# Kernel tuning notes

Hardware: AMD Instinct MI355X
Metric: run time of the kernel (lower is better)

Reference implementation:

```python
import jax, jax.numpy as jnp
import numpy as np

N_NODES = 20000
N_EDGES = 100000
WALK_LEN = 4
FEAT_DIM = 256
HID = 64
NUM_HEAD = 8
H_RNN = NUM_HEAD * HID  # 512
OUT_DIM = 16


def setup_inputs() -> dict:
    key = jax.random.key(0)
    ks = jax.random.split(key, 12)
    s = 0.05  # small init scale for numerical stability
    return {
        "x": jax.random.normal(ks[0], (N_NODES, FEAT_DIM), jnp.float32),
        "W_mlp": jax.random.normal(ks[1], (HID, FEAT_DIM), jnp.float32) * s,
        "b_mlp": jnp.zeros((HID,), jnp.float32),
        "W_ih": jax.random.normal(ks[2], (3 * H_RNN, HID), jnp.float32) * s,
        "W_hh": jax.random.normal(ks[3], (3 * H_RNN, H_RNN), jnp.float32) * s,
        "b_ih": jnp.zeros((3 * H_RNN,), jnp.float32),
        "b_hh": jnp.zeros((3 * H_RNN,), jnp.float32),
        "attn": jax.random.normal(ks[4], (1, NUM_HEAD, HID), jnp.float32) * s,
        "W_emb": jax.random.normal(ks[5], (HID, H_RNN), jnp.float32) * s,
        "b_emb": jnp.zeros((HID,), jnp.float32),
        "W_last": jax.random.normal(ks[6], (OUT_DIM, HID), jnp.float32) * s,
        "b_last": jnp.zeros((OUT_DIM,), jnp.float32),
        "edge_metapath_indices": jax.random.randint(ks[7], (N_EDGES, WALK_LEN), 0, N_NODES),
        "num_nodes": N_NODES,
    }


def reference(x, W_mlp, b_mlp, W_ih, W_hh, b_ih, b_hh, attn, W_emb, b_emb,
              W_last, b_last, edge_metapath_indices, num_nodes):
    # self channel: embedding = mlp(data.x)
    emb = x @ W_mlp.T + b_mlp                       # [N, hid]

    # rnn channel: gather per-metapath node embeddings
    edata = emb[edge_metapath_indices]              # [E, L, hid]
    E = edata.shape[0]
    h_rnn = W_hh.shape[1]

    # torch nn.GRU cell (gate order r, z, n), scan over path length
    def gru_step(h, x_t):
        xg = x_t @ W_ih.T + b_ih                    # [E, 3H]
        hg = h @ W_hh.T + b_hh                      # [E, 3H]
        xr, xz, xn = jnp.split(xg, 3, axis=-1)
        hr, hz, hn = jnp.split(hg, 3, axis=-1)
        r = jax.nn.sigmoid(xr + hr)
        z = jax.nn.sigmoid(xz + hz)
        n = jnp.tanh(xn + r * hn)
        return (1.0 - z) * n + z * h, None

    h0 = jnp.zeros((E, h_rnn), edata.dtype)
    hT, _ = jax.lax.scan(gru_step, h0, jnp.swapaxes(edata, 0, 1))  # [E, 8*hid]

    num_head, hid = attn.shape[1], attn.shape[2]
    eft = hT.reshape(E, num_head, hid)              # per-edge features

    # attention logits + leaky_relu(0.01)
    a = jnp.sum(eft * attn, axis=-1)                # [E, num_head]
    a = jnp.where(a > 0, a, 0.01 * a)

    # edge softmax grouped by destination node (indices[:, -1])
    dst = edge_metapath_indices[:, -1]
    m = jax.ops.segment_max(a, dst, num_segments=num_nodes)        # [N, H]
    ea = jnp.exp(a - m[dst])
    ssum = jax.ops.segment_sum(ea, dst, num_segments=num_nodes)    # [N, H]
    alpha = ea / ssum[dst]                          # [E, H]

    # message passing: scatter-sum of attention-weighted edge features
    ft = jax.ops.segment_sum(eft * alpha[:, :, None], dst,
                             num_segments=num_nodes)               # [N, H, hid]
    ret = ft.reshape(num_nodes, num_head * hid)
    rnn_emb = ret @ W_emb.T + b_emb                 # [N, hid]

    out = rnn_emb @ W_last.T + b_last               # [N, out_dim]
    return out
```

## Files before the change

### kernel.cpp

```cpp
#include <hip/hip_runtime.h>
#include <hip/hip_bf16.h>
#include <cstdint>

#define N_NODES 20000
#define N_EDGES 100000
#define WALK 4
#define FDIM 256
#define HID 64
#define NHEAD 8
#define HR 512
#define OUTD 16

typedef __attribute__((ext_vector_type(8))) short bf16x8;
typedef __attribute__((ext_vector_type(8))) unsigned short u16x8;
typedef __attribute__((ext_vector_type(4))) float f32x4;

__device__ __forceinline__ float b2f(unsigned short u){
  union{float f; unsigned u;} x; x.u = ((unsigned)u)<<16; return x.f;
}
__device__ __forceinline__ unsigned short f2b(float f){
  union{float f; unsigned u;} x; x.f = f;
  unsigned r = x.u + 0x7FFFu + ((x.u>>16)&1u);
  return (unsigned short)(r>>16);
}
__device__ __forceinline__ float sigmoidf_(float v){ return 1.0f/(1.0f+__expf(-v)); }
__device__ __forceinline__ float tanh_c(float v){
  v = fminf(fmaxf(v, -15.f), 15.f);
  const float t2 = __expf(2.0f*v);
  return (t2 - 1.0f) / (t2 + 1.0f);
}

__device__ __forceinline__ void gload16(const void* g, void* l){
  __builtin_amdgcn_global_load_lds(
      (const __attribute__((address_space(1))) void*)(g),
      (__attribute__((address_space(3))) void*)(l),
      16, 0, 0);
}

__device__ __forceinline__ f32x4 mfma16(bf16x8 a, bf16x8 b, f32x4 c){
  return __builtin_amdgcn_mfma_f32_16x16x32_bf16(a, b, c, 0, 0, 0);
}

__launch_bounds__(256)
__global__ void emb_kernel(const float* __restrict__ x,
                           const float* __restrict__ Wm,
                           const float* __restrict__ bm,
                           unsigned short* __restrict__ emb_bf)
{
  __shared__ float xs[4][FDIM];
  const int tid = threadIdx.x;
  const int node0 = blockIdx.x * 4;
  {
    const int row = tid >> 6;
    const int k4  = (tid & 63) * 4;
    *reinterpret_cast<float4*>(&xs[row][k4]) =
      *reinterpret_cast<const float4*>(&x[(size_t)(node0+row)*FDIM + k4]);
  }
  __syncthreads();
  const int nn = tid >> 6, c = tid & 63;
  float acc = bm[c];
  const float* wr = &Wm[c*FDIM];
  #pragma unroll 8
  for (int k=0;k<FDIM;k+=4){
    const float4 w = *reinterpret_cast<const float4*>(&wr[k]);
    acc += xs[nn][k]*w.x + xs[nn][k+1]*w.y + xs[nn][k+2]*w.z + xs[nn][k+3]*w.w;
  }
  emb_bf[(size_t)(node0+nn)*HID + c] = f2b(acc);
}

__launch_bounds__(256)
__global__ void prep_kernel(const float* __restrict__ Whh,
                            const float* __restrict__ Wih,
                            const float* __restrict__ Wemb,
                            unsigned short* __restrict__ WhhP,
                            unsigned short* __restrict__ WihP,
                            unsigned short* __restrict__ WembP)
{
  const int t = blockIdx.x*256 + threadIdx.x;
  if (t < 8*192*512){
    const int k = t & 511;
    const int r = (t >> 9) % 192;
    const int db = t / 98304;
    const int G = (r>>6)*HR + db*64 + (r&63);
    const int kg = k >> 6, kw = k & 63;
    const int c = kw >> 3, o = kw & 7;
    const int ksrc = (kg<<6) + (((c ^ (r&7)) << 3) | o);
    WhhP[t] = f2b(Whh[(size_t)G*HR + ksrc]);
  }
  if (t < 8*192*64){
    const int k = t & 63;
    const int r = (t >> 6) % 192;
    const int db = t / 12288;
    const int G = (r>>6)*HR + db*64 + (r&63);
    const int c = k >> 3, o = k & 7;
    const int ksrc = (((c ^ (r&7)) << 3) | o);
    WihP[t] = f2b(Wih[(size_t)G*HID + ksrc]);
  }
  if (t < 64*512){
    const int k = t & 511;
    const int o = t >> 9;
    const int kg = k >> 6, kw = k & 63;
    const int c = kw >> 3, off = kw & 7;
    const int ksrc = (kg<<6) + (((c ^ (o&7)) << 3) | off);
    WembP[t] = f2b(Wemb[(size_t)o*HR + ksrc]);
  }
}

__launch_bounds__(256)
__global__ void xg_kernel(const unsigned short* __restrict__ emb_bf,
                          const unsigned short* __restrict__ WihP,
                          const float* __restrict__ b_ih,
                          const float* __restrict__ b_hh,
                          unsigned short* __restrict__ xnP,
                          unsigned short* __restrict__ h1n)
{
  __shared__ __align__(16) unsigned short As[128*64];
  __shared__ __align__(16) unsigned short Bs[192*64];
  const int tid = threadIdx.x, lane = tid & 63, w = tid >> 6;
  const int tx = lane & 15, ty = lane >> 4;
  const int n0 = blockIdx.x * 128;
  const int db = blockIdx.y;

  #pragma unroll
  for (int j=0;j<4;++j){
    const int flat = j*256 + tid;
    const int row = flat >> 3, c = flat & 7;
    int n = n0 + row; if (n > N_NODES-1) n = N_NODES-1;
    gload16(emb_bf + ((size_t)n*HID + ((c ^ (row&7))<<3)), (char*)As + flat*16);
  }
  #pragma unroll
  for (int j=0;j<6;++j){
    const int flat = j*256 + tid;
    const int row = flat >> 3, c = flat & 7;
    gload16(WihP + ((size_t)(db*192 + row)*HID + c*8), (char*)Bs + flat*16);
  }
  __syncthreads();

  f32x4 acc[2][12];
  #pragma unroll
  for (int m=0;m<2;++m)
    #pragma unroll
    for (int f=0;f<12;++f) acc[m][f] = (f32x4)(0.f);

  auto readFrag = [&](const unsigned short* base, int row, int kk)->bf16x8{
    const int chunk = (kk<<2) + ty;
    return *reinterpret_cast<const bf16x8*>(
        reinterpret_cast<const char*>(base) + (row<<7) + ((chunk ^ (row&7))<<4));
  };
  #pragma unroll
  for (int kk=0; kk<2; ++kk){
    const bf16x8 a0 = readFrag(As, w*32 + tx, kk);
    const bf16x8 a1 = readFrag(As, w*32 + 16 + tx, kk);
    #pragma unroll
    for (int nf=0; nf<12; ++nf){
      const bf16x8 b = readFrag(Bs, nf*16 + tx, kk);
      acc[0][nf] = mfma16(a0, b, acc[0][nf]);
      acc[1][nf] = mfma16(a1, b, acc[1][nf]);
    }
  }

  #pragma unroll
  for (int m=0;m<2;++m){
    #pragma unroll
    for (int reg=0; reg<4; ++reg){
      const int row = w*32 + m*16 + ty*4 + reg;
      const int n = n0 + row;
      if (n < N_NODES){
        #pragma unroll
        for (int fr=0; fr<4; ++fr){
          const int d6 = fr*16 + tx;
          const int dG = db*64 + d6;
          const float xr = acc[m][fr][reg]   + b_ih[dG];
          const float xz = acc[m][4+fr][reg] + b_ih[HR+dG];
          const float xn = acc[m][8+fr][reg] + b_ih[2*HR+dG];
          xnP[((size_t)db*N_NODES + n)*64 + d6] = f2b(xn);
          const float r = sigmoidf_(xr + b_hh[dG]);
          const float z = sigmoidf_(xz + b_hh[HR+dG]);
          const float nn = tanh_c(xn + r*b_hh[2*HR+dG]);
          h1n[(size_t)n*HR + dG] = f2b((1.0f - z)*nn);
        }
      }
    }
  }
}

template<int STEP, bool SCORE>
__launch_bounds__(256)
__global__ void gru_mfma(const unsigned short* __restrict__ emb_bf,
                         const int* __restrict__ idx,
                         const unsigned short* __restrict__ h_in,
                         unsigned short* __restrict__ h_out,
                         const unsigned short* __restrict__ WhhP,
                         const unsigned short* __restrict__ WihP,
                         const unsigned short* __restrict__ xnP,
                         const float* __restrict__ b_ih,
                         const float* __restrict__ b_hh,
                         const float* __restrict__ attn,
                         float* __restrict__ a_buf)
{
  constexpr bool GATHER = (STEP == 1);
  __shared__ __align__(16) unsigned short As[128*64];
  __shared__ __align__(16) unsigned short Bs[192*64];

  const int tid = threadIdx.x, lane = tid & 63, w = tid >> 6;
  const int tx = lane & 15, ty = lane >> 4;

  const int bid = blockIdx.x;
  const int sid = (bid & 7)*782 + (bid >> 3);
  const int et = sid >> 3;
  const int db = sid & 7;
  const int e0 = et * 128;

  int eS[4], nH[4], nX[4];
  #pragma unroll
  for (int j=0;j<4;++j){
    int e = e0 + ((j*256 + tid) >> 3);
    if (e > N_EDGES-1) e = N_EDGES-1;
    eS[j] = e;
    nX[j] = idx[e*WALK + STEP];
    nH[j] = GATHER ? idx[e*WALK] : 0;
  }

  f32x4 acc[2][12];
  #pragma unroll
  for (int m=0;m<2;++m)
    #pragma unroll
    for (int f=0;f<12;++f) acc[m][f] = (f32x4)(0.f);

  auto stageA = [&](int kt){
    #pragma unroll
    for (int j=0;j<4;++j){
      const int flat = j*256 + tid;
      const int row = flat >> 3, c = flat & 7;
      const unsigned short* src;
      if (kt == 8){
        src = emb_bf + ((size_t)nX[j]*HID + ((c ^ (row&7)) << 3));
      } else if (GATHER){
        src = h_in + ((size_t)nH[j]*HR + kt*64 + ((c ^ (row&7)) << 3));
      } else {
        src = h_in + ((size_t)eS[j]*HR + kt*64 + c*8);
      }
      gload16(src, (char*)As + flat*16);
    }
  };
  auto stageB = [&](int kt){
    #pragma unroll
    for (int j=0;j<6;++j){
      const int flat = j*256 + tid;
      const int row = flat >> 3, c = flat & 7;
      const unsigned short* src = (kt < 8)
        ? WhhP + ((size_t)(db*192 + row)*HR + kt*64 + c*8)
        : WihP + ((size_t)(db*192 + row)*HID + c*8);
      gload16(src, (char*)Bs + flat*16);
    }
  };
  auto readFrag = [&](const unsigned short* base, int row, int kk)->bf16x8{
    const int chunk = (kk<<2) + ty;
    return *reinterpret_cast<const bf16x8*>(
        reinterpret_cast<const char*>(base) + (row<<7) + ((chunk ^ (row&7))<<4));
  };

  stageA(0); stageB(0);

  #pragma unroll
  for (int kt=0; kt<9; ++kt){
    __syncthreads();
    #pragma unroll
    for (int kk=0; kk<2; ++kk){
      const bf16x8 a0 = readFrag(As, w*32 + tx, kk);
      const bf16x8 a1 = readFrag(As, w*32 + 16 + tx, kk);
      #pragma unroll
      for (int nf=0; nf<12; ++nf){
        if (kt == 8 && nf >= 8) continue;
        const bf16x8 b = readFrag(Bs, nf*16 + tx, kk);
        acc[0][nf] = mfma16(a0, b, acc[0][nf]);
        acc[1][nf] = mfma16(a1, b, acc[1][nf]);
      }
    }
    if (kt < 8){
      __syncthreads();
      stageA(kt+1); stageB(kt+1);
    }
  }

  float bir[4], biz[4], bhn[4], atv[4];
  #pragma unroll
  for (int fr=0; fr<4; ++fr){
    const int dG = db*64 + fr*16 + tx;
    bir[fr] = b_ih[dG]      + b_hh[dG];
    biz[fr] = b_ih[HR+dG]   + b_hh[HR+dG];
    bhn[fr] = b_hh[2*HR+dG];
    atv[fr] = SCORE ? attn[dG] : 0.f;
  }

  #pragma unroll
  for (int m=0;m<2;++m){
    #pragma unroll
    for (int reg=0; reg<4; ++reg){
      const int row = w*32 + m*16 + ty*4 + reg;
      const int e = e0 + row;
      float sp = 0.f;
      if (e < N_EDGES){
        const int nodeS = idx[e*WALK + STEP];
        const int nodeH = GATHER ? idx[e*WALK] : 0;
        #pragma unroll
        for (int fr=0; fr<4; ++fr){
          const int d6 = fr*16 + tx;
          const int dG = db*64 + d6;
          const float xn = b2f(xnP[((size_t)db*N_NODES + nodeS)*64 + d6]);
          float hold;
          if (GATHER) hold = b2f(h_in[(size_t)nodeH*HR + dG]);
          else        hold = b2f(h_in[(size_t)e*HR + db*64 + (((d6>>3) ^ (e&7))<<3) + (d6&7)]);
          const float r  = sigmoidf_(acc[m][fr][reg]   + bir[fr]);
          const float z  = sigmoidf_(acc[m][4+fr][reg] + biz[fr]);
          const float nn = tanh_c(xn + r*(acc[m][8+fr][reg] + bhn[fr]));
          const float hv = (1.0f - z)*nn + z*hold;
          h_out[(size_t)e*HR + db*64 + (((d6>>3) ^ (e&7))<<3) + (d6&7)] = f2b(hv);
          if (SCORE) sp += hv * atv[fr];
        }
      }
      if (SCORE){
        sp += __shfl_xor(sp, 1);
        sp += __shfl_xor(sp, 2);
        sp += __shfl_xor(sp, 4);
        sp += __shfl_xor(sp, 8);
        if (tx == 0 && e < N_EDGES) a_buf[e*NHEAD + db] = sp;
      }
    }
  }
}

__launch_bounds__(256)
__global__ void score2_kernel(const int* __restrict__ idx,
                              float* __restrict__ a_buf,
                              unsigned int* __restrict__ mmax)
{
  const int flat = blockIdx.x*256 + threadIdx.x;
  const int e = flat >> 3, h = flat & 7;
  const float s = a_buf[flat];
  const float a = s > 0.f ? s : 0.01f*s;
  a_buf[flat] = a;
  const int dst = idx[e*WALK + 3];
  union{float f; unsigned u;} x; x.f = a;
  const unsigned key = (x.u & 0x80000000u) ? ~x.u : (x.u | 0x80000000u);
  atomicMax(&mmax[dst*NHEAD + h], key);
}

__launch_bounds__(256)
__global__ void ea_kernel(const int* __restrict__ idx,
                          float* __restrict__ a_buf,
                          const unsigned int* __restrict__ mmax,
                          float* __restrict__ ssum)
{
  const int flat = blockIdx.x*256 + threadIdx.x;
  const int e = flat >> 3, h = flat & 7;
  const int dst = idx[e*WALK + 3];
  const unsigned key = mmax[dst*NHEAD + h];
  union{float f; unsigned u;} x;
  x.u = (key & 0x80000000u) ? (key & 0x7FFFFFFFu) : ~key;
  const float ea = __expf(a_buf[flat] - x.f);
  a_buf[flat] = ea;
  atomicAdd(&ssum[dst*NHEAD + h], ea);
}

__launch_bounds__(256)
__global__ void z_kernel(const unsigned short* __restrict__ hT,
                         const int* __restrict__ idx,
                         const float* __restrict__ ea_buf,
                         const float* __restrict__ ssum,
                         const unsigned short* __restrict__ WembP,
                         float* __restrict__ zacc)
{
  __shared__ __align__(16) char zs[40960];
  char* Az = zs;
  char* Bz = zs + 32768;
  const int tid = threadIdx.x;
  const int lane = tid & 63;
  const int w = tid >> 6;
  const int e0 = blockIdx.x * 256;

  int ej[8], dstj[8];
  #pragma unroll
  for (int j=0;j<8;++j){
    int e = e0 + ((j*256 + tid) >> 3);
    if (e > N_EDGES-1) e = N_EDGES-1;
    ej[j] = e;
    dstj[j] = idx[e*WALK + 3];
  }

  f32x4 acc[4][4];
  #pragma unroll
  for (int m=0;m<4;++m)
    #pragma unroll
    for (int f=0;f<4;++f) acc[m][f] = (f32x4)(0.f);

  auto readFrag = [&](const char* base, int row, int kk)->bf16x8{
    const int chunk = (kk<<2) + (lane>>4);
    return *reinterpret_cast<const bf16x8*>(base + (row<<7) + ((chunk ^ (row&7))<<4));
  };

  #pragma unroll 1
  for (int kt=0; kt<8; ++kt){
    __syncthreads();
    #pragma unroll
    for (int j=0;j<8;++j){
      const int flat = j*256 + tid;
      const int e = ej[j];
      const u16x8 hv = *reinterpret_cast<const u16x8*>(hT + (size_t)e*HR + kt*64 + (flat&7)*8);
      const float al = ea_buf[e*NHEAD + kt] / ssum[dstj[j]*NHEAD + kt];
      union { bf16x8 v; unsigned short s[8]; } o;
      #pragma unroll
      for (int i=0;i<8;++i) o.s[i] = f2b(b2f(hv[i]) * al);
      *reinterpret_cast<bf16x8*>(Az + flat*16) = o.v;
    }
    #pragma unroll
    for (int j=0;j<2;++j){
      const int flat = j*256 + tid;
      const int row = flat >> 3, c = flat & 7;
      gload16(WembP + ((size_t)row*HR + kt*64 + c*8), Bz + ((j*256 + w*64)<<4));
    }
    __syncthreads();
    #pragma unroll
    for (int kk=0; kk<2; ++kk){
      bf16x8 a_[4];
      #pragma unroll
      for (int mf=0; mf<4; ++mf)
        a_[mf] = readFrag(Az, w*64 + mf*16 + (lane&15), kk);
      #pragma unroll
      for (int nf=0; nf<4; ++nf){
        const bf16x8 b_ = readFrag(Bz, nf*16 + (lane&15), kk);
        #pragma unroll
        for (int mf=0; mf<4; ++mf)
          acc[mf][nf] = mfma16(a_[mf], b_, acc[mf][nf]);
      }
    }
  }

  #pragma unroll
  for (int mf=0; mf<4; ++mf){
    #pragma unroll
    for (int reg=0; reg<4; ++reg){
      const int row = w*64 + mf*16 + ((lane>>4)<<2) + reg;
      const int e = e0 + row;
      if (e < N_EDGES){
        const int dst = idx[e*WALK + 3];
        #pragma unroll
        for (int nf=0; nf<4; ++nf){
          const int o = nf*16 + (lane&15);
          atomicAdd(&zacc[(size_t)dst*64 + o], acc[mf][nf][reg]);
        }
      }
    }
  }
}

__launch_bounds__(256)
__global__ void out2_kernel(const float* __restrict__ zacc,
                            const float* __restrict__ b_emb,
                            const float* __restrict__ W_last,
                            const float* __restrict__ b_last,
                            float* __restrict__ out)
{
  const int flat = blockIdx.x*256 + threadIdx.x;
  if (flat >= N_NODES*OUTD) return;
  const int n = flat >> 4, o = flat & 15;
  float s = b_last[o];
  const float* zr = &zacc[(size_t)n*64];
  const float* wl = &W_last[o*64];
  #pragma unroll
  for (int k=0;k<64;++k) s += (zr[k] + b_emb[k]) * wl[k];
  out[(size_t)n*OUTD + o] = s;
}

extern "C" void kernel_launch(void* const* d_in, const int* in_sizes, int n_in,
                              void* d_out, int out_size, void* d_ws, size_t ws_size,
                              hipStream_t stream)
{
  (void)in_sizes; (void)n_in; (void)out_size; (void)ws_size;
  const float* x      = (const float*)d_in[0];
  const float* W_mlp  = (const float*)d_in[1];
  const float* b_mlp  = (const float*)d_in[2];
  const float* W_ih   = (const float*)d_in[3];
  const float* W_hh   = (const float*)d_in[4];
  const float* b_ih   = (const float*)d_in[5];
  const float* b_hh   = (const float*)d_in[6];
  const float* attn   = (const float*)d_in[7];
  const float* W_emb  = (const float*)d_in[8];
  const float* b_emb  = (const float*)d_in[9];
  const float* W_last = (const float*)d_in[10];
  const float* b_last = (const float*)d_in[11];
  const int*   idx    = (const int*)d_in[12];
  float* out = (float*)d_out;

  char* ws = (char*)d_ws;
  unsigned short* WhhP   = (unsigned short*)(ws + 0);
  unsigned short* WihP   = (unsigned short*)(ws + 1572864);
  unsigned short* WembP  = (unsigned short*)(ws + 1769472);
  unsigned short* emb_bf = (unsigned short*)(ws + 1835008);
  unsigned short* xnP    = (unsigned short*)(ws + 4395008);
  float*          a_buf  = (float*)(ws + 24875008);
  unsigned int*   mmax   = (unsigned int*)(ws + 28075008);
  float*          ssum   = (float*)(ws + 28715008);
  float*          zacc   = (float*)(ws + 29355008);
  unsigned short* h_a    = (unsigned short*)(ws + 34475008);
  unsigned short* h_b    = (unsigned short*)(ws + 136875008);
  unsigned short* h1n    = h_b;

  hipMemsetAsync(a_buf, 0, 9600000, stream);

  prep_kernel<<<3072, 256, 0, stream>>>(W_hh, W_ih, W_emb, WhhP, WihP, WembP);
  emb_kernel<<<N_NODES/4, 256, 0, stream>>>(x, W_mlp, b_mlp, emb_bf);

  dim3 xgrid((N_NODES + 127)/128, 8);
  xg_kernel<<<xgrid, 256, 0, stream>>>(emb_bf, WihP, b_ih, b_hh, xnP, h1n);

  const int NWG = 782*8;
  gru_mfma<1,false><<<NWG, 256, 0, stream>>>(emb_bf, idx, h1n, h_a, WhhP, WihP, xnP, b_ih, b_hh, attn, a_buf);
  gru_mfma<2,false><<<NWG, 256, 0, stream>>>(emb_bf, idx, h_a, h_b, WhhP, WihP, xnP, b_ih, b_hh, attn, a_buf);
  gru_mfma<3,true ><<<NWG, 256, 0, stream>>>(emb_bf, idx, h_b, h_a, WhhP, WihP, xnP, b_ih, b_hh, attn, a_buf);

  score2_kernel<<<N_EDGES*NHEAD/256, 256, 0, stream>>>(idx, a_buf, mmax);
  ea_kernel<<<N_EDGES*NHEAD/256, 256, 0, stream>>>(idx, a_buf, mmax, ssum);
  z_kernel<<<391, 256, 0, stream>>>(h_a, idx, a_buf, ssum, WembP, zacc);
  out2_kernel<<<(N_NODES*OUTD+255)/256, 256, 0, stream>>>(zacc, b_emb, W_last, b_last, out);
}
```

Baseline: 1.184 ms.

## Reorder gate weight rows and retile GRU MFMA to 2x2 wave grid

Permutes packed W_hh/W_ih rows so that each 16-row fragment group interleaves the r, z and n gates for the same hidden slice. The GRU step kernels then split the 128x192 tile across waves as 2x2 (64 rows by 96 columns) instead of 4x1, which cuts redundant B-fragment LDS reads per wave. The attention partial score is now accumulated with atomicAdd because two waves each contribute half of the head's dot product. xg_kernel moves to 512 threads with 256-node tiles. The cost is extra atomics and higher register pressure from the 4x6 accumulator layout.

```diff
diff --git a/kernel.cpp b/kernel.cpp
--- a/kernel.cpp
+++ b/kernel.cpp
@@ -81,7 +81,9 @@
     const int k = t & 511;
     const int r = (t >> 9) % 192;
     const int db = t / 98304;
-    const int G = (r>>6)*HR + db*64 + (r&63);
+    const int f = r >> 4, fr = r & 15;
+    const int g = f % 3, dgrp = f / 3;
+    const int G = g*HR + db*64 + dgrp*16 + fr;
     const int kg = k >> 6, kw = k & 63;
     const int c = kw >> 3, o = kw & 7;
     const int ksrc = (kg<<6) + (((c ^ (r&7)) << 3) | o);
@@ -91,7 +93,9 @@
     const int k = t & 63;
     const int r = (t >> 6) % 192;
     const int db = t / 12288;
-    const int G = (r>>6)*HR + db*64 + (r&63);
+    const int f = r >> 4, fr = r & 15;
+    const int g = f % 3, dgrp = f / 3;
+    const int G = g*HR + db*64 + dgrp*16 + fr;
     const int c = k >> 3, o = k & 7;
     const int ksrc = (((c ^ (r&7)) << 3) | o);
     WihP[t] = f2b(Wih[(size_t)G*HID + ksrc]);
@@ -106,7 +110,7 @@
   }
 }
 
-__launch_bounds__(256)
+__launch_bounds__(512)
 __global__ void xg_kernel(const unsigned short* __restrict__ emb_bf,
                           const unsigned short* __restrict__ WihP,
                           const float* __restrict__ b_ih,
@@ -114,65 +118,68 @@
                           unsigned short* __restrict__ xnP,
                           unsigned short* __restrict__ h1n)
 {
-  __shared__ __align__(16) unsigned short As[128*64];
-  __shared__ __align__(16) unsigned short Bs[192*64];
+  __shared__ __align__(16) char smem[32768 + 24576];
+  char* Ab = smem;
+  char* Bb = smem + 32768;
   const int tid = threadIdx.x, lane = tid & 63, w = tid >> 6;
-  const int tx = lane & 15, ty = lane >> 4;
-  const int n0 = blockIdx.x * 128;
+  const int wr = w >> 1, wn = w & 1;
+  const int n0 = blockIdx.x * 256;
   const int db = blockIdx.y;
 
   #pragma unroll
   for (int j=0;j<4;++j){
-    const int flat = j*256 + tid;
+    const int flat = j*512 + tid;
     const int row = flat >> 3, c = flat & 7;
     int n = n0 + row; if (n > N_NODES-1) n = N_NODES-1;
-    gload16(emb_bf + ((size_t)n*HID + ((c ^ (row&7))<<3)), (char*)As + flat*16);
-  }
-  #pragma unroll
-  for (int j=0;j<6;++j){
-    const int flat = j*256 + tid;
+    gload16(emb_bf + ((size_t)n*HID + ((c ^ (row&7))<<3)), Ab + ((j*512 + w*64)<<4));
+  }
+  #pragma unroll
+  for (int j=0;j<3;++j){
+    const int flat = j*512 + tid;
     const int row = flat >> 3, c = flat & 7;
-    gload16(WihP + ((size_t)(db*192 + row)*HID + c*8), (char*)Bs + flat*16);
-  }
-  __syncthreads();
-
-  f32x4 acc[2][12];
-  #pragma unroll
-  for (int m=0;m<2;++m)
-    #pragma unroll
-    for (int f=0;f<12;++f) acc[m][f] = (f32x4)(0.f);
-
-  auto readFrag = [&](const unsigned short* base, int row, int kk)->bf16x8{
-    const int chunk = (kk<<2) + ty;
-    return *reinterpret_cast<const bf16x8*>(
-        reinterpret_cast<const char*>(base) + (row<<7) + ((chunk ^ (row&7))<<4));
+    gload16(WihP + ((size_t)(db*192 + row)*HID + c*8), Bb + ((j*512 + w*64)<<4));
+  }
+  asm volatile("s_waitcnt vmcnt(0)" ::: "memory");
+  __builtin_amdgcn_s_barrier();
+
+  f32x4 acc[4][6];
+  #pragma unroll
+  for (int m=0;m<4;++m)
+    #pragma unroll
+    for (int f=0;f<6;++f) acc[m][f] = (f32x4)(0.f);
+
+  auto readFrag = [&](const char* base, int row, int kk)->bf16x8{
+    const int chunk = (kk<<2) + (lane>>4);
+    return *reinterpret_cast<const bf16x8*>(base + (row<<7) + ((chunk ^ (row&7))<<4));
   };
   #pragma unroll
   for (int kk=0; kk<2; ++kk){
-    const bf16x8 a0 = readFrag(As, w*32 + tx, kk);
-    const bf16x8 a1 = readFrag(As, w*32 + 16 + tx, kk);
-    #pragma unroll
-    for (int nf=0; nf<12; ++nf){
-      const bf16x8 b = readFrag(Bs, nf*16 + tx, kk);
-      acc[0][nf] = mfma16(a0, b, acc[0][nf]);
-      acc[1][nf] = mfma16(a1, b, acc[1][nf]);
-    }
-  }
-
-  #pragma unroll
-  for (int m=0;m<2;++m){
+    bf16x8 a_[4];
+    #pragma unroll
+    for (int mf=0; mf<4; ++mf) a_[mf] = readFrag(Ab, wr*64 + mf*16 + (lane&15), kk);
+    #pragma unroll
+    for (int nf=0; nf<6; ++nf){
+      const bf16x8 b_ = readFrag(Bb, wn*96 + nf*16 + (lane&15), kk);
+      #pragma unroll
+      for (int mf=0; mf<4; ++mf) acc[mf][nf] = mfma16(a_[mf], b_, acc[mf][nf]);
+    }
+  }
+
+  const int fr_ = lane & 15;
+  #pragma unroll
+  for (int mf=0; mf<4; ++mf){
     #pragma unroll
     for (int reg=0; reg<4; ++reg){
-      const int row = w*32 + m*16 + ty*4 + reg;
+      const int row = wr*64 + mf*16 + ((lane>>4)<<2) + reg;
       const int n = n0 + row;
       if (n < N_NODES){
         #pragma unroll
-        for (int fr=0; fr<4; ++fr){
-          const int d6 = fr*16 + tx;
+        for (int t=0; t<2; ++t){
+          const int d6 = (2*wn+t)*16 + fr_;
           const int dG = db*64 + d6;
-          const float xr = acc[m][fr][reg]   + b_ih[dG];
-          const float xz = acc[m][4+fr][reg] + b_ih[HR+dG];
-          const float xn = acc[m][8+fr][reg] + b_ih[2*HR+dG];
+          const float xr = acc[mf][t*3+0][reg] + b_ih[dG];
+          const float xz = acc[mf][t*3+1][reg] + b_ih[HR+dG];
+          const float xn = acc[mf][t*3+2][reg] + b_ih[2*HR+dG];
           xnP[((size_t)db*N_NODES + n)*64 + d6] = f2b(xn);
           const float r = sigmoidf_(xr + b_hh[dG]);
           const float z = sigmoidf_(xz + b_hh[HR+dG]);
@@ -204,6 +211,7 @@
 
   const int tid = threadIdx.x, lane = tid & 63, w = tid >> 6;
   const int tx = lane & 15, ty = lane >> 4;
+  const int wm = w >> 1, wn = w & 1;
 
   const int bid = blockIdx.x;
   const int sid = (bid & 7)*782 + (bid >> 3);
@@ -221,11 +229,11 @@
     nH[j] = GATHER ? idx[e*WALK] : 0;
   }
 
-  f32x4 acc[2][12];
-  #pragma unroll
-  for (int m=0;m<2;++m)
-    #pragma unroll
-    for (int f=0;f<12;++f) acc[m][f] = (f32x4)(0.f);
+  f32x4 acc[4][6];
+  #pragma unroll
+  for (int m=0;m<4;++m)
+    #pragma unroll
+    for (int f=0;f<6;++f) acc[m][f] = (f32x4)(0.f);
 
   auto stageA = [&](int kt){
     #pragma unroll
@@ -267,14 +275,17 @@
     __syncthreads();
     #pragma unroll
     for (int kk=0; kk<2; ++kk){
-      const bf16x8 a0 = readFrag(As, w*32 + tx, kk);
-      const bf16x8 a1 = readFrag(As, w*32 + 16 + tx, kk);
+      bf16x8 a_[4];
       #pragma unroll
-      for (int nf=0; nf<12; ++nf){
-        if (kt == 8 && nf >= 8) continue;
-        const bf16x8 b = readFrag(Bs, nf*16 + tx, kk);
-        acc[0][nf] = mfma16(a0, b, acc[0][nf]);
-        acc[1][nf] = mfma16(a1, b, acc[1][nf]);
+      for (int mf=0; mf<4; ++mf)
+        a_[mf] = readFrag(As, wm*64 + mf*16 + tx, kk);
+      #pragma unroll
+      for (int nf=0; nf<6; ++nf){
+        if (kt == 8 && (nf % 3) == 2) continue;
+        const bf16x8 b = readFrag(Bs, wn*96 + nf*16 + tx, kk);
+        #pragma unroll
+        for (int mf=0; mf<4; ++mf)
+          acc[mf][nf] = mfma16(a_[mf], b, acc[mf][nf]);
       }
     }
     if (kt < 8){
@@ -283,40 +294,40 @@
     }
   }
 
-  float bir[4], biz[4], bhn[4], atv[4];
-  #pragma unroll
-  for (int fr=0; fr<4; ++fr){
-    const int dG = db*64 + fr*16 + tx;
-    bir[fr] = b_ih[dG]      + b_hh[dG];
-    biz[fr] = b_ih[HR+dG]   + b_hh[HR+dG];
-    bhn[fr] = b_hh[2*HR+dG];
-    atv[fr] = SCORE ? attn[dG] : 0.f;
-  }
-
-  #pragma unroll
-  for (int m=0;m<2;++m){
+  float bir[2], biz[2], bhn[2], atv[2];
+  #pragma unroll
+  for (int t=0; t<2; ++t){
+    const int dG = db*64 + (2*wn+t)*16 + tx;
+    bir[t] = b_ih[dG]      + b_hh[dG];
+    biz[t] = b_ih[HR+dG]   + b_hh[HR+dG];
+    bhn[t] = b_hh[2*HR+dG];
+    atv[t] = SCORE ? attn[dG] : 0.f;
+  }
+
+  #pragma unroll
+  for (int mf=0; mf<4; ++mf){
     #pragma unroll
     for (int reg=0; reg<4; ++reg){
-      const int row = w*32 + m*16 + ty*4 + reg;
+      const int row = wm*64 + mf*16 + ty*4 + reg;
       const int e = e0 + row;
       float sp = 0.f;
       if (e < N_EDGES){
         const int nodeS = idx[e*WALK + STEP];
         const int nodeH = GATHER ? idx[e*WALK] : 0;
         #pragma unroll
-        for (int fr=0; fr<4; ++fr){
-          const int d6 = fr*16 + tx;
+        for (int t=0; t<2; ++t){
+          const int d6 = (2*wn+t)*16 + tx;
           const int dG = db*64 + d6;
           const float xn = b2f(xnP[((size_t)db*N_NODES + nodeS)*64 + d6]);
           float hold;
           if (GATHER) hold = b2f(h_in[(size_t)nodeH*HR + dG]);
           else        hold = b2f(h_in[(size_t)e*HR + db*64 + (((d6>>3) ^ (e&7))<<3) + (d6&7)]);
-          const float r  = sigmoidf_(acc[m][fr][reg]   + bir[fr]);
-          const float z  = sigmoidf_(acc[m][4+fr][reg] + biz[fr]);
-          const float nn = tanh_c(xn + r*(acc[m][8+fr][reg] + bhn[fr]));
+          const float r  = sigmoidf_(acc[mf][t*3+0][reg] + bir[t]);
+          const float z  = sigmoidf_(acc[mf][t*3+1][reg] + biz[t]);
+          const float nn = tanh_c(xn + r*(acc[mf][t*3+2][reg] + bhn[t]));
           const float hv = (1.0f - z)*nn + z*hold;
           h_out[(size_t)e*HR + db*64 + (((d6>>3) ^ (e&7))<<3) + (d6&7)] = f2b(hv);
-          if (SCORE) sp += hv * atv[fr];
+          if (SCORE) sp += hv * atv[t];
         }
       }
       if (SCORE){
@@ -324,7 +335,8 @@
         sp += __shfl_xor(sp, 2);
         sp += __shfl_xor(sp, 4);
         sp += __shfl_xor(sp, 8);
-        if (tx == 0 && e < N_EDGES) a_buf[e*NHEAD + db] = sp;
+        if (tx == 0 && e < N_EDGES)
+          atomicAdd(&a_buf[e*NHEAD + db], sp);
       }
     }
   }
@@ -511,8 +523,8 @@
   prep_kernel<<<3072, 256, 0, stream>>>(W_hh, W_ih, W_emb, WhhP, WihP, WembP);
   emb_kernel<<<N_NODES/4, 256, 0, stream>>>(x, W_mlp, b_mlp, emb_bf);
 
-  dim3 xgrid((N_NODES + 127)/128, 8);
-  xg_kernel<<<xgrid, 256, 0, stream>>>(emb_bf, WihP, b_ih, b_hh, xnP, h1n);
+  dim3 xgrid(79, 8);
+  xg_kernel<<<xgrid, 512, 0, stream>>>(emb_bf, WihP, b_ih, b_hh, xnP, h1n);
 
   const int NWG = 782*8;
   gru_mfma<1,false><<<NWG, 256, 0, stream>>>(emb_bf, idx, h1n, h_a, WhhP, WihP, xnP, b_ih, b_hh, attn, a_buf);
```

Result: slower. 1.299 ms (+9.7%).

## Double GRU edge tile to 256 with 512 threads and fuse score/max into GRU

Applied to the files above, without the earlier changes.

The GRU MFMA kernel now runs 512-thread blocks that each cover 256 edges instead of 128. Each block stages the same 192-row weight tile once for twice as many edges, which halves redundant weight loads per edge. The separate score2 kernel is removed: the last GRU step applies leaky_relu and does the atomicMax into mmax directly, and the memset now clears only mmax and ssum. The cost is higher LDS and register pressure per block, and the compute loop (hidden) must handle the doubled rows correctly; there is also a risk that mmax and ssum are no longer both zeroed if the layout differs.

```diff
diff --git a/kernel.cpp b/kernel.cpp
--- a/kernel.cpp
+++ b/kernel.cpp
@@ -185,7 +185,7 @@
 }
 
 template<int STEP, bool SCORE>
-__launch_bounds__(256)
+__launch_bounds__(512, 2)
 __global__ void gru_mfma(const unsigned short* __restrict__ emb_bf,
                          const int* __restrict__ idx,
                          const unsigned short* __restrict__ h_in,
@@ -196,25 +196,26 @@
                          const float* __restrict__ b_ih,
                          const float* __restrict__ b_hh,
                          const float* __restrict__ attn,
-                         float* __restrict__ a_buf)
+                         float* __restrict__ a_buf,
+                         unsigned int* __restrict__ mmax)
 {
   constexpr bool GATHER = (STEP == 1);
-  __shared__ __align__(16) unsigned short As[128*64];
+  __shared__ __align__(16) unsigned short As[256*64];
   __shared__ __align__(16) unsigned short Bs[192*64];
 
   const int tid = threadIdx.x, lane = tid & 63, w = tid >> 6;
   const int tx = lane & 15, ty = lane >> 4;
 
   const int bid = blockIdx.x;
-  const int sid = (bid & 7)*782 + (bid >> 3);
+  const int sid = (bid & 7)*391 + (bid >> 3);
   const int et = sid >> 3;
   const int db = sid & 7;
-  const int e0 = et * 128;
+  const int e0 = et * 256;
 
   int eS[4], nH[4], nX[4];
   #pragma unroll
   for (int j=0;j<4;++j){
-    int e = e0 + ((j*256 + tid) >> 3);
+    int e = e0 + ((j*512 + tid) >> 3);
     if (e > N_EDGES-1) e = N_EDGES-1;
     eS[j] = e;
     nX[j] = idx[e*WALK + STEP];
@@ -230,7 +231,7 @@
   auto stageA = [&](int kt){
     #pragma unroll
     for (int j=0;j<4;++j){
-      const int flat = j*256 + tid;
+      const int flat = j*512 + tid;
       const int row = flat >> 3, c = flat & 7;
       const unsigned short* src;
       if (kt == 8){
@@ -245,8 +246,8 @@
   };
   auto stageB = [&](int kt){
     #pragma unroll
-    for (int j=0;j<6;++j){
-      const int flat = j*256 + tid;
+    for (int j=0;j<3;++j){
+      const int flat = j*512 + tid;
       const int row = flat >> 3, c = flat & 7;
       const unsigned short* src = (kt < 8)
         ? WhhP + ((size_t)(db*192 + row)*HR + kt*64 + c*8)
@@ -324,26 +325,17 @@
         sp += __shfl_xor(sp, 2);
         sp += __shfl_xor(sp, 4);
         sp += __shfl_xor(sp, 8);
-        if (tx == 0 && e < N_EDGES) a_buf[e*NHEAD + db] = sp;
-      }
-    }
-  }
-}
-
-__launch_bounds__(256)
-__global__ void score2_kernel(const int* __restrict__ idx,
-                              float* __restrict__ a_buf,
-                              unsigned int* __restrict__ mmax)
-{
-  const int flat = blockIdx.x*256 + threadIdx.x;
-  const int e = flat >> 3, h = flat & 7;
-  const float s = a_buf[flat];
-  const float a = s > 0.f ? s : 0.01f*s;
-  a_buf[flat] = a;
-  const int dst = idx[e*WALK + 3];
-  union{float f; unsigned u;} x; x.f = a;
-  const unsigned key = (x.u & 0x80000000u) ? ~x.u : (x.u | 0x80000000u);
-  atomicMax(&mmax[dst*NHEAD + h], key);
+        if (tx == 0 && e < N_EDGES){
+          const float a = sp > 0.f ? sp : 0.01f*sp;
+          a_buf[e*NHEAD + db] = a;
+          const int dst = idx[e*WALK + 3];
+          union{float f; unsigned u;} xx; xx.f = a;
+          const unsigned key = (xx.u & 0x80000000u) ? ~xx.u : (xx.u | 0x80000000u);
+          atomicMax(&mmax[dst*NHEAD + db], key);
+        }
+      }
+    }
+  }
 }
 
 __launch_bounds__(256)
@@ -506,7 +498,7 @@
   unsigned short* h_b    = (unsigned short*)(ws + 136875008);
   unsigned short* h1n    = h_b;
 
-  hipMemsetAsync(a_buf, 0, 9600000, stream);
+  hipMemsetAsync(mmax, 0, 6400000, stream);
 
   prep_kernel<<<3072, 256, 0, stream>>>(W_hh, W_ih, W_emb, WhhP, WihP, WembP);
   emb_kernel<<<N_NODES/4, 256, 0, stream>>>(x, W_mlp, b_mlp, emb_bf);
@@ -514,12 +506,11 @@
   dim3 xgrid((N_NODES + 127)/128, 8);
   xg_kernel<<<xgrid, 256, 0, stream>>>(emb_bf, WihP, b_ih, b_hh, xnP, h1n);
 
-  const int NWG = 782*8;
-  gru_mfma<1,false><<<NWG, 256, 0, stream>>>(emb_bf, idx, h1n, h_a, WhhP, WihP, xnP, b_ih, b_hh, attn, a_buf);
-  gru_mfma<2,false><<<NWG, 256, 0, stream>>>(emb_bf, idx, h_a, h_b, WhhP, WihP, xnP, b_ih, b_hh, attn, a_buf);
-  gru_mfma<3,true ><<<NWG, 256, 0, stream>>>(emb_bf, idx, h_b, h_a, WhhP, WihP, xnP, b_ih, b_hh, attn, a_buf);
-
-  score2_kernel<<<N_EDGES*NHEAD/256, 256, 0, stream>>>(idx, a_buf, mmax);
+  const int NWG = 391*8;
+  gru_mfma<1,false><<<NWG, 512, 0, stream>>>(emb_bf, idx, h1n, h_a, WhhP, WihP, xnP, b_ih, b_hh, attn, a_buf, mmax);
+  gru_mfma<2,false><<<NWG, 512, 0, stream>>>(emb_bf, idx, h_a, h_b, WhhP, WihP, xnP, b_ih, b_hh, attn, a_buf, mmax);
+  gru_mfma<3,true ><<<NWG, 512, 0, stream>>>(emb_bf, idx, h_b, h_a, WhhP, WihP, xnP, b_ih, b_hh, attn, a_buf, mmax);
+
   ea_kernel<<<N_EDGES*NHEAD/256, 256, 0, stream>>>(idx, a_buf, mmax, ssum);
   z_kernel<<<391, 256, 0, stream>>>(h_a, idx, a_buf, ssum, WembP, zacc);
   out2_kernel<<<(N_NODES*OUTD+255)/256, 256, 0, stream>>>(zacc, b_emb, W_last, b_last, out);
```

New measurement: 1.307 ms. 1.1x slower.

## Precompute per-node hidden gate projections for GRU step one and fuse score into step three

Applied to the files above, without the earlier changes.

The step-1 hidden state depends only on the first node, so W_hh·h1 is now computed once per node (20000 rows) in a new hgn kernel, not once per edge (100000 rows). A lighter step1x kernel then does only the 64-wide input GEMM and gathers the precomputed gate values. Separately, the leaky-relu and the atomicMax for the segment max move into the step-3 epilogue, which removes score2_kernel, and the memset now clears mmax/ssum instead of a_buf. The cost is an extra bf16 rounding of the hidden-gate projections and a new per-node buffer.

```diff
diff --git a/kernel.cpp b/kernel.cpp
--- a/kernel.cpp
+++ b/kernel.cpp
@@ -184,6 +184,183 @@
   }
 }
 
+__launch_bounds__(256)
+__global__ void hgn_kernel(const unsigned short* __restrict__ h1n,
+                           const unsigned short* __restrict__ WhhP,
+                           unsigned short* __restrict__ hgP)
+{
+  __shared__ __align__(16) unsigned short As[128*64];
+  __shared__ __align__(16) unsigned short Bs[192*64];
+  const int tid = threadIdx.x, lane = tid & 63, w = tid >> 6;
+  const int tx = lane & 15, ty = lane >> 4;
+  const int n0 = blockIdx.x * 128;
+  const int db = blockIdx.y;
+
+  f32x4 acc[2][12];
+  #pragma unroll
+  for (int m=0;m<2;++m)
+    #pragma unroll
+    for (int f=0;f<12;++f) acc[m][f] = (f32x4)(0.f);
+
+  auto stageA = [&](int kt){
+    #pragma unroll
+    for (int j=0;j<4;++j){
+      const int flat = j*256 + tid;
+      const int row = flat >> 3, c = flat & 7;
+      int n = n0 + row; if (n > N_NODES-1) n = N_NODES-1;
+      gload16(h1n + ((size_t)n*HR + kt*64 + ((c ^ (row&7)) << 3)), (char*)As + flat*16);
+    }
+  };
+  auto stageB = [&](int kt){
+    #pragma unroll
+    for (int j=0;j<6;++j){
+      const int flat = j*256 + tid;
+      const int row = flat >> 3, c = flat & 7;
+      gload16(WhhP + ((size_t)(db*192 + row)*HR + kt*64 + c*8), (char*)Bs + flat*16);
+    }
+  };
+  auto readFrag = [&](const unsigned short* base, int row, int kk)->bf16x8{
+    const int chunk = (kk<<2) + ty;
+    return *reinterpret_cast<const bf16x8*>(
+        reinterpret_cast<const char*>(base) + (row<<7) + ((chunk ^ (row&7))<<4));
+  };
+
+  stageA(0); stageB(0);
+  #pragma unroll
+  for (int kt=0; kt<8; ++kt){
+    __syncthreads();
+    #pragma unroll
+    for (int kk=0; kk<2; ++kk){
+      const bf16x8 a0 = readFrag(As, w*32 + tx, kk);
+      const bf16x8 a1 = readFrag(As, w*32 + 16 + tx, kk);
+      #pragma unroll
+      for (int nf=0; nf<12; ++nf){
+        const bf16x8 b = readFrag(Bs, nf*16 + tx, kk);
+        acc[0][nf] = mfma16(a0, b, acc[0][nf]);
+        acc[1][nf] = mfma16(a1, b, acc[1][nf]);
+      }
+    }
+    if (kt < 7){
+      __syncthreads();
+      stageA(kt+1); stageB(kt+1);
+    }
+  }
+
+  #pragma unroll
+  for (int m=0;m<2;++m){
+    #pragma unroll
+    for (int reg=0; reg<4; ++reg){
+      const int row = w*32 + m*16 + ty*4 + reg;
+      const int n = n0 + row;
+      if (n < N_NODES){
+        #pragma unroll
+        for (int nf=0; nf<12; ++nf)
+          hgP[((size_t)db*N_NODES + n)*192 + nf*16 + tx] = f2b(acc[m][nf][reg]);
+      }
+    }
+  }
+}
+
+__launch_bounds__(256)
+__global__ void step1x_kernel(const unsigned short* __restrict__ emb_bf,
+                              const int* __restrict__ idx,
+                              const unsigned short* __restrict__ h1n,
+                              const unsigned short* __restrict__ hgP,
+                              const unsigned short* __restrict__ xnP,
+                              const unsigned short* __restrict__ WihP,
+                              unsigned short* __restrict__ h_out,
+                              const float* __restrict__ b_ih,
+                              const float* __restrict__ b_hh)
+{
+  __shared__ __align__(16) unsigned short As[128*64];
+  __shared__ __align__(16) unsigned short Bs[128*64];
+  const int tid = threadIdx.x, lane = tid & 63, w = tid >> 6;
+  const int tx = lane & 15, ty = lane >> 4;
+
+  const int bid = blockIdx.x;
+  const int sid = (bid & 7)*782 + (bid >> 3);
+  const int et = sid >> 3;
+  const int db = sid & 7;
+  const int e0 = et * 128;
+
+  #pragma unroll
+  for (int j=0;j<4;++j){
+    const int flat = j*256 + tid;
+    const int row = flat >> 3, c = flat & 7;
+    int e = e0 + row; if (e > N_EDGES-1) e = N_EDGES-1;
+    const int n1 = idx[e*WALK + 1];
+    gload16(emb_bf + ((size_t)n1*HID + ((c ^ (row&7)) << 3)), (char*)As + flat*16);
+  }
+  #pragma unroll
+  for (int j=0;j<4;++j){
+    const int flat = j*256 + tid;
+    const int row = flat >> 3, c = flat & 7;
+    gload16(WihP + ((size_t)(db*192 + row)*HID + c*8), (char*)Bs + flat*16);
+  }
+  __syncthreads();
+
+  f32x4 acc[2][8];
+  #pragma unroll
+  for (int m=0;m<2;++m)
+    #pragma unroll
+    for (int f=0;f<8;++f) acc[m][f] = (f32x4)(0.f);
+
+  auto readFrag = [&](const unsigned short* base, int row, int kk)->bf16x8{
+    const int chunk = (kk<<2) + ty;
+    return *reinterpret_cast<const bf16x8*>(
+        reinterpret_cast<const char*>(base) + (row<<7) + ((chunk ^ (row&7))<<4));
+  };
+  #pragma unroll
+  for (int kk=0; kk<2; ++kk){
+    const bf16x8 a0 = readFrag(As, w*32 + tx, kk);
+    const bf16x8 a1 = readFrag(As, w*32 + 16 + tx, kk);
+    #pragma unroll
+    for (int nf=0; nf<8; ++nf){
+      const bf16x8 b = readFrag(Bs, nf*16 + tx, kk);
+      acc[0][nf] = mfma16(a0, b, acc[0][nf]);
+      acc[1][nf] = mfma16(a1, b, acc[1][nf]);
+    }
+  }
+
+  float bir[4], biz[4], bhn[4];
+  #pragma unroll
+  for (int fr=0; fr<4; ++fr){
+    const int dG = db*64 + fr*16 + tx;
+    bir[fr] = b_ih[dG]      + b_hh[dG];
+    biz[fr] = b_ih[HR+dG]   + b_hh[HR+dG];
+    bhn[fr] = b_hh[2*HR+dG];
+  }
+
+  #pragma unroll
+  for (int m=0;m<2;++m){
+    #pragma unroll
+    for (int reg=0; reg<4; ++reg){
+      const int row = w*32 + m*16 + ty*4 + reg;
+      const int e = e0 + row;
+      if (e < N_EDGES){
+        const int n0 = idx[e*WALK];
+        const int n1 = idx[e*WALK + 1];
+        const size_t hb = ((size_t)db*N_NODES + n0)*192;
+        #pragma unroll
+        for (int fr=0; fr<4; ++fr){
+          const int d6 = fr*16 + tx;
+          const int dG = db*64 + d6;
+          const float hr = b2f(hgP[hb + d6]);
+          const float hz = b2f(hgP[hb + 64 + d6]);
+          const float hn = b2f(hgP[hb + 128 + d6]) + bhn[fr];
+          const float xn = b2f(xnP[((size_t)db*N_NODES + n1)*64 + d6]);
+          const float hold = b2f(h1n[(size_t)n0*HR + dG]);
+          const float r  = sigmoidf_(acc[m][fr][reg]   + hr + bir[fr]);
+          const float z  = sigmoidf_(acc[m][4+fr][reg] + hz + biz[fr]);
+          const float nn = tanh_c(xn + r*hn);
+          const float hv = (1.0f - z)*nn + z*hold;
+          h_out[(size_t)e*HR + db*64 + (((d6>>3) ^ (e&7))<<3) + (d6&7)] = f2b(hv);
+        }
+      }
+    }
+  }
+}
+
 template<int STEP, bool SCORE>
 __launch_bounds__(256)
 __global__ void gru_mfma(const unsigned short* __restrict__ emb_bf,
@@ -196,9 +373,9 @@
                          const float* __restrict__ b_ih,
                          const float* __restrict__ b_hh,
                          const float* __restrict__ attn,
-                         float* __restrict__ a_buf)
-{
-  constexpr bool GATHER = (STEP == 1);
+                         float* __restrict__ a_buf,
+                         unsigned int* __restrict__ mmax)
+{
   __shared__ __align__(16) unsigned short As[128*64];
   __shared__ __align__(16) unsigned short Bs[192*64];
 
@@ -211,14 +388,13 @@
   const int db = sid & 7;
   const int e0 = et * 128;
 
-  int eS[4], nH[4], nX[4];
+  int eS[4], nX[4];
   #pragma unroll
   for (int j=0;j<4;++j){
     int e = e0 + ((j*256 + tid) >> 3);
     if (e > N_EDGES-1) e = N_EDGES-1;
     eS[j] = e;
     nX[j] = idx[e*WALK + STEP];
-    nH[j] = GATHER ? idx[e*WALK] : 0;
   }
 
   f32x4 acc[2][12];
@@ -235,8 +411,6 @@
       const unsigned short* src;
       if (kt == 8){
         src = emb_bf + ((size_t)nX[j]*HID + ((c ^ (row&7)) << 3));
-      } else if (GATHER){
-        src = h_in + ((size_t)nH[j]*HR + kt*64 + ((c ^ (row&7)) << 3));
       } else {
         src = h_in + ((size_t)eS[j]*HR + kt*64 + c*8);
       }
@@ -302,15 +476,11 @@
       float sp = 0.f;
       if (e < N_EDGES){
         const int nodeS = idx[e*WALK + STEP];
-        const int nodeH = GATHER ? idx[e*WALK] : 0;
         #pragma unroll
         for (int fr=0; fr<4; ++fr){
           const int d6 = fr*16 + tx;
-          const int dG = db*64 + d6;
           const float xn = b2f(xnP[((size_t)db*N_NODES + nodeS)*64 + d6]);
-          float hold;
-          if (GATHER) hold = b2f(h_in[(size_t)nodeH*HR + dG]);
-          else        hold = b2f(h_in[(size_t)e*HR + db*64 + (((d6>>3) ^ (e&7))<<3) + (d6&7)]);
+          const float hold = b2f(h_in[(size_t)e*HR + db*64 + (((d6>>3) ^ (e&7))<<3) + (d6&7)]);
           const float r  = sigmoidf_(acc[m][fr][reg]   + bir[fr]);
           const float z  = sigmoidf_(acc[m][4+fr][reg] + biz[fr]);
           const float nn = tanh_c(xn + r*(acc[m][8+fr][reg] + bhn[fr]));
@@ -324,26 +494,17 @@
         sp += __shfl_xor(sp, 2);
         sp += __shfl_xor(sp, 4);
         sp += __shfl_xor(sp, 8);
-        if (tx == 0 && e < N_EDGES) a_buf[e*NHEAD + db] = sp;
-      }
-    }
-  }
-}
-
-__launch_bounds__(256)
-__global__ void score2_kernel(const int* __restrict__ idx,
-                              float* __restrict__ a_buf,
-                              unsigned int* __restrict__ mmax)
-{
-  const int flat = blockIdx.x*256 + threadIdx.x;
-  const int e = flat >> 3, h = flat & 7;
-  const float s = a_buf[flat];
-  const float a = s > 0.f ? s : 0.01f*s;
-  a_buf[flat] = a;
-  const int dst = idx[e*WALK + 3];
-  union{float f; unsigned u;} x; x.f = a;
-  const unsigned key = (x.u & 0x80000000u) ? ~x.u : (x.u | 0x80000000u);
-  atomicMax(&mmax[dst*NHEAD + h], key);
+        if (tx == 0 && e < N_EDGES){
+          const float a = sp > 0.f ? sp : 0.01f*sp;
+          a_buf[e*NHEAD + db] = a;
+          const int dst = idx[e*WALK + 3];
+          union{float f; unsigned u;} xx; xx.f = a;
+          const unsigned key = (xx.u & 0x80000000u) ? ~xx.u : (xx.u | 0x80000000u);
+          atomicMax(&mmax[dst*NHEAD + db], key);
+        }
+      }
+    }
+  }
 }
 
 __launch_bounds__(256)
@@ -505,21 +666,22 @@
   unsigned short* h_a    = (unsigned short*)(ws + 34475008);
   unsigned short* h_b    = (unsigned short*)(ws + 136875008);
   unsigned short* h1n    = h_b;
-
-  hipMemsetAsync(a_buf, 0, 9600000, stream);
+  unsigned short* hgP    = (unsigned short*)(ws + 157355008);
+
+  (void)hipMemsetAsync(mmax, 0, 6400000, stream);
 
   prep_kernel<<<3072, 256, 0, stream>>>(W_hh, W_ih, W_emb, WhhP, WihP, WembP);
   emb_kernel<<<N_NODES/4, 256, 0, stream>>>(x, W_mlp, b_mlp, emb_bf);
 
-  dim3 xgrid((N_NODES + 127)/128, 8);
-  xg_kernel<<<xgrid, 256, 0, stream>>>(emb_bf, WihP, b_ih, b_hh, xnP, h1n);
+  dim3 ngrid((N_NODES + 127)/128, 8);
+  xg_kernel<<<ngrid, 256, 0, stream>>>(emb_bf, WihP, b_ih, b_hh, xnP, h1n);
+  hgn_kernel<<<ngrid, 256, 0, stream>>>(h1n, WhhP, hgP);
 
   const int NWG = 782*8;
-  gru_mfma<1,false><<<NWG, 256, 0, stream>>>(emb_bf, idx, h1n, h_a, WhhP, WihP, xnP, b_ih, b_hh, attn, a_buf);
-  gru_mfma<2,false><<<NWG, 256, 0, stream>>>(emb_bf, idx, h_a, h_b, WhhP, WihP, xnP, b_ih, b_hh, attn, a_buf);
-  gru_mfma<3,true ><<<NWG, 256, 0, stream>>>(emb_bf, idx, h_b, h_a, WhhP, WihP, xnP, b_ih, b_hh, attn, a_buf);
-
-  score2_kernel<<<N_EDGES*NHEAD/256, 256, 0, stream>>>(idx, a_buf, mmax);
+  step1x_kernel<<<NWG, 256, 0, stream>>>(emb_bf, idx, h1n, hgP, xnP, WihP, h_a, b_ih, b_hh);
+  gru_mfma<2,false><<<NWG, 256, 0, stream>>>(emb_bf, idx, h_a, h_b, WhhP, WihP, xnP, b_ih, b_hh, attn, a_buf, mmax);
+  gru_mfma<3,true ><<<NWG, 256, 0, stream>>>(emb_bf, idx, h_b, h_a, WhhP, WihP, xnP, b_ih, b_hh, attn, a_buf, mmax);
+
   ea_kernel<<<N_EDGES*NHEAD/256, 256, 0, stream>>>(idx, a_buf, mmax, ssum);
   z_kernel<<<391, 256, 0, stream>>>(h_a, idx, a_buf, ssum, WembP, zacc);
   out2_kernel<<<(N_NODES*OUTD+255)/256, 256, 0, stream>>>(zacc, b_emb, W_last, b_last, out);
```

Measured after the change: 1.170 ms. About the same (-1.2%).
